# Performance work log

Measured on AMD Instinct MI355X. Metric: run time of the kernel, lower is better.

## Reference

```python
import jax, jax.numpy as jnp
import numpy as np

B, L, D = 16384, 50, 32  # batch, history length, embedding_dim
NU, NI, NC = 100000, 100000, 1000


def setup_inputs() -> dict:
    key = jax.random.key(0)
    ks = jax.random.split(key, 16)
    customer_id = jax.random.randint(ks[0], (B,), 0, NU)
    candidate_good = jax.random.randint(ks[1], (B,), 0, NI)
    candidate_class = jax.random.randint(ks[2], (B,), 0, NC)
    history_goods = jax.random.randint(ks[3], (B, L), 0, NI)
    history_classes = jax.random.randint(ks[4], (B, L), 0, NC)
    user_table = jax.random.normal(ks[5], (NU, D), jnp.float32) * 0.05
    item_table = jax.random.normal(ks[6], (NI, D), jnp.float32) * 0.05
    item_table = item_table.at[0].set(0.0)  # padding_idx=0
    cat_table = jax.random.normal(ks[7], (NC, D), jnp.float32) * 0.05
    cat_table = cat_table.at[0].set(0.0)  # padding_idx=0
    # attention net: Linear(4*2D=256 -> 80), Linear(80 -> 1)
    aw1 = jax.random.normal(ks[8], (4 * 2 * D, 80), jnp.float32) * 0.05
    ab1 = jnp.zeros((80,), jnp.float32)
    aw2 = jax.random.normal(ks[9], (80, 1), jnp.float32) * 0.05
    ab2 = jnp.zeros((1,), jnp.float32)
    # final mlp: 5D=160 -> 256 -> 128 -> 1
    mw1 = jax.random.normal(ks[10], (5 * D, 256), jnp.float32) * 0.05
    mb1 = jnp.zeros((256,), jnp.float32)
    mw2 = jax.random.normal(ks[11], (256, 128), jnp.float32) * 0.05
    mb2 = jnp.zeros((128,), jnp.float32)
    mw3 = jax.random.normal(ks[12], (128, 1), jnp.float32) * 0.05
    mb3 = jnp.zeros((1,), jnp.float32)
    return dict(customer_id=customer_id, candidate_good=candidate_good,
                candidate_class=candidate_class, history_goods=history_goods,
                history_classes=history_classes, user_table=user_table,
                item_table=item_table, cat_table=cat_table,
                aw1=aw1, ab1=ab1, aw2=aw2, ab2=ab2,
                mw1=mw1, mb1=mb1, mw2=mw2, mb2=mb2, mw3=mw3, mb3=mb3)


def reference(customer_id, candidate_good, candidate_class, history_goods,
              history_classes, user_table, item_table, cat_table,
              aw1, ab1, aw2, ab2, mw1, mb1, mw2, mb2, mw3, mb3):
    user_emb = user_table[customer_id]                               # [B, D]
    cand = jnp.concatenate([item_table[candidate_good],
                            cat_table[candidate_class]], axis=-1)    # [B, 2D]
    hist = jnp.concatenate([item_table[history_goods],
                            cat_table[history_classes]], axis=-1)    # [B, L, 2D]
    q = jnp.broadcast_to(cand[:, None, :], hist.shape)               # [B, L, 2D]
    info = jnp.concatenate([q, hist, q - hist, q * hist], axis=-1)   # [B, L, 8D]
    h = jax.nn.relu(info @ aw1 + ab1)                                # [B, L, 80]
    scores = (h @ aw2 + ab2)[..., 0]                                 # [B, L]
    mask = history_goods != 0
    scores = jnp.where(mask, scores, -1e9)
    weights = jax.nn.softmax(scores, axis=1)                         # [B, L]
    att = jnp.einsum('bl,bld->bd', weights, hist)                    # [B, 2D]
    combined = jnp.concatenate([user_emb, cand, att], axis=-1)       # [B, 5D]
    z = jax.nn.relu(combined @ mw1 + mb1)
    z = jax.nn.relu(z @ mw2 + mb2)
    out = (z @ mw3 + mb3)[..., 0]                                    # [B]
    return out
```

## Files before the change

### kernel.cpp

```cpp
#include <hip/hip_runtime.h>
#include <math.h>

#define LHIST 50

typedef __attribute__((ext_vector_type(8))) short bf16x8;
typedef __attribute__((ext_vector_type(4))) float f32x4;

__device__ __forceinline__ unsigned short f2bf(float f) {
    union { float f; unsigned u; } v; v.f = f;
    unsigned r = v.u + 0x7fff + ((v.u >> 16) & 1);
    return (unsigned short)(r >> 16);
}
__device__ __forceinline__ float bf2f(unsigned short h) {
    union { unsigned u; float f; } v; v.u = ((unsigned)h) << 16;
    return v.f;
}


__global__ void prep_kernel(const float* __restrict__ aw1,
                            const float* __restrict__ mw1,
                            const float* __restrict__ mw2,
                            const float* __restrict__ item_table,
                            const float* __restrict__ cat_table,
                            int itemN, int catN,
                            float* __restrict__ Awt,
                            unsigned short* __restrict__ Bmfb,
                            unsigned short* __restrict__ W4fb,
                            unsigned short* __restrict__ W1f,
                            unsigned short* __restrict__ W2f,
                            unsigned short* __restrict__ itemb,
                            unsigned short* __restrict__ catb) {
    int i = blockIdx.x * 256 + threadIdx.x;
    int i8 = i * 8;
    if (i8 + 7 < itemN) {
        float4 a = *(const float4*)&item_table[i8];
        float4 b = *(const float4*)&item_table[i8 + 4];
        ushort4 lo, hi;
        lo.x = f2bf(a.x); lo.y = f2bf(a.y); lo.z = f2bf(a.z); lo.w = f2bf(a.w);
        hi.x = f2bf(b.x); hi.y = f2bf(b.y); hi.z = f2bf(b.z); hi.w = f2bf(b.w);
        *(ushort4*)&itemb[i8] = lo;
        *(ushort4*)&itemb[i8 + 4] = hi;
    }
    if (i8 + 7 < catN) {
        float4 a = *(const float4*)&cat_table[i8];
        float4 b = *(const float4*)&cat_table[i8 + 4];
        ushort4 lo, hi;
        lo.x = f2bf(a.x); lo.y = f2bf(a.y); lo.z = f2bf(a.z); lo.w = f2bf(a.w);
        hi.x = f2bf(b.x); hi.y = f2bf(b.y); hi.z = f2bf(b.z); hi.w = f2bf(b.w);
        *(ushort4*)&catb[i8] = lo;
        *(ushort4*)&catb[i8 + 4] = hi;
    }
    if (i < 5120) {
        int j = i >> 6, k = i & 63;
        Awt[i] = aw1[k * 80 + j] + aw1[(128 + k) * 80 + j];
        int kk = i / 80, n = i - kk * 80;
        int nt = n >> 4, colw = n & 15, ks = kk >> 5, r = kk & 31, qd = r >> 3, off = r & 7;
        int d = ((nt * 2 + ks) * 64 + qd * 16 + colw) * 8 + off;
        Bmfb[d] = f2bf(aw1[(64 + kk) * 80 + n] - aw1[(128 + kk) * 80 + n]);
        W4fb[d] = f2bf(aw1[(192 + kk) * 80 + n]);
    }
    if (i < 40960) {
        int kk = i >> 8, n = i & 255;
        int nt = n >> 4, colw = n & 15, ks = kk >> 5, r = kk & 31, qd = r >> 3, off = r & 7;
        W1f[((nt * 5 + ks) * 64 + qd * 16 + colw) * 8 + off] = f2bf(mw1[i]);
    }
    if (i < 32768) {
        int kk = i >> 7, n = i & 127;
        int nt = n >> 4, colw = n & 15, ks = kk >> 5, r = kk & 31, qd = r >> 3, off = r & 7;
        W2f[((nt * 8 + ks) * 64 + qd * 16 + colw) * 8 + off] = f2bf(mw2[i]);
    }
}

__device__ __forceinline__ bf16x8 hq_frag(uint4 v, const float* qp) {
    union { uint4 u; unsigned short s[8]; } in; in.u = v;
    bf16x8 r;
    #pragma unroll
    for (int j = 0; j < 8; ++j) r[j] = (short)f2bf(bf2f(in.s[j]) * qp[j]);
    return r;
}

__global__ void __launch_bounds__(256, 4) attn_kernel(
    const int* __restrict__ cid, const int* __restrict__ cg,
    const int* __restrict__ cc,  const int* __restrict__ hg,
    const int* __restrict__ hc,
    const float* __restrict__ user_table, const float* __restrict__ item_table,
    const float* __restrict__ cat_table,
    const float* __restrict__ ab1, const float* __restrict__ aw2,
    const float* __restrict__ Awt, const unsigned short* __restrict__ Bmfb,
    const unsigned short* __restrict__ W4fb,
    const unsigned short* __restrict__ itemb, const unsigned short* __restrict__ catb,
    unsigned short* __restrict__ cfrag)
{
    __shared__ __align__(16) unsigned short sh_B[20 * 64 * 8];
    __shared__ __align__(16) float sh_q[4][64];
    __shared__ float sh_bias[4][80];
    __shared__ float sh_sc[4][64];
    __shared__ float sh_aw2[80];

    const int t = threadIdx.x;
    const int b0 = blockIdx.x * 4;
    const int wv = t >> 6;
    const int lane = t & 63;
    const int quad = lane >> 4;
    const int col = lane & 15;

    for (int i = t; i < 1280; i += 256) {
        int lane8 = i & 63;
        int ksnt = i >> 6;
        int nt = ksnt >> 2, ks = ksnt & 3;
        const unsigned short* src = (ks < 2)
            ? &Bmfb[((nt * 2 + ks) * 64 + lane8) * 8]
            : &W4fb[((nt * 2 + (ks - 2)) * 64 + lane8) * 8];
        *(uint4*)&sh_B[i * 8] = *(const uint4*)src;
    }
    {
        int qbi = wv;
        int b = b0 + qbi;
        float v = (lane < 32) ? item_table[(size_t)cg[b] * 32 + lane]
                              : cat_table[(size_t)cc[b] * 32 + (lane - 32)];
        sh_q[qbi][lane] = v;
    }
    if (t < 80) sh_aw2[t] = aw2[t];
    __syncthreads();

    const int b = b0 + wv;

    int il[4], ic[4];
    #pragma unroll
    for (int mt = 0; mt < 4; ++mt) {
        int l = mt * 16 + col;
        int lc = (l < LHIST) ? l : 0;
        il[mt] = hg[b * LHIST + lc];
        ic[mt] = hc[b * LHIST + lc];
    }
    uint4 vi0 = *(const uint4*)&itemb[(size_t)il[0] * 32 + quad * 8];
    uint4 vc0 = *(const uint4*)&catb[(size_t)ic[0] * 32 + quad * 8];
    uint4 vi1 = *(const uint4*)&itemb[(size_t)il[1] * 32 + quad * 8];
    uint4 vc1 = *(const uint4*)&catb[(size_t)ic[1] * 32 + quad * 8];

    for (int s = t; s < 320; s += 256) {
        int bi = s / 80, j = s - bi * 80;
        float acc = ab1[j];
        const float4* aw = (const float4*)&Awt[j * 64];
        #pragma unroll
        for (int k4 = 0; k4 < 16; ++k4) {
            float4 a = aw[k4];
            float4 q = *(const float4*)&sh_q[bi][k4 * 4];
            acc += a.x * q.x + a.y * q.y + a.z * q.z + a.w * q.w;
        }
        sh_bias[bi][j] = acc;
    }
    __syncthreads();

    float q0[8], q1[8];
    {
        float4 qa = *(const float4*)&sh_q[wv][quad * 8];
        float4 qb = *(const float4*)&sh_q[wv][quad * 8 + 4];
        q0[0]=qa.x; q0[1]=qa.y; q0[2]=qa.z; q0[3]=qa.w; q0[4]=qb.x; q0[5]=qb.y; q0[6]=qb.z; q0[7]=qb.w;
        float4 qc = *(const float4*)&sh_q[wv][32 + quad * 8];
        float4 qdv = *(const float4*)&sh_q[wv][32 + quad * 8 + 4];
        q1[0]=qc.x; q1[1]=qc.y; q1[2]=qc.z; q1[3]=qc.w; q1[4]=qdv.x; q1[5]=qdv.y; q1[6]=qdv.z; q1[7]=qdv.w;
    }
    float bias_v[5], a2_v[5];
    #pragma unroll
    for (int nt = 0; nt < 5; ++nt) {
        bias_v[nt] = sh_bias[wv][nt * 16 + col];
        a2_v[nt]   = sh_aw2[nt * 16 + col];
    }

    #pragma unroll
    for (int p = 0; p < 2; ++p) {
        bf16x8 afr[2][4];
        uint4 vi[2], vc[2];
        if (p == 0) { vi[0] = vi0; vc[0] = vc0; vi[1] = vi1; vc[1] = vc1; }
        else {
            vi[0] = *(const uint4*)&itemb[(size_t)il[2] * 32 + quad * 8];
            vc[0] = *(const uint4*)&catb[(size_t)ic[2] * 32 + quad * 8];
            vi[1] = *(const uint4*)&itemb[(size_t)il[3] * 32 + quad * 8];
            vc[1] = *(const uint4*)&catb[(size_t)ic[3] * 32 + quad * 8];
            if (48 + col >= LHIST) { vi[1] = make_uint4(0,0,0,0); vc[1] = make_uint4(0,0,0,0); }
        }
        #pragma unroll
        for (int mi = 0; mi < 2; ++mi) {
            afr[mi][0] = *(bf16x8*)&vi[mi];
            afr[mi][1] = *(bf16x8*)&vc[mi];
            afr[mi][2] = hq_frag(vi[mi], q0);
            afr[mi][3] = hq_frag(vc[mi], q1);
        }
        f32x4 acc[2][5];
        #pragma unroll
        for (int mi = 0; mi < 2; ++mi)
            #pragma unroll
            for (int nt = 0; nt < 5; ++nt) acc[mi][nt] = (f32x4){0.f,0.f,0.f,0.f};
        #pragma unroll
        for (int ks = 0; ks < 4; ++ks) {
            #pragma unroll
            for (int nt = 0; nt < 5; ++nt) {
                bf16x8 bfr = *(const bf16x8*)&sh_B[((nt * 4 + ks) * 64 + lane) * 8];
                acc[0][nt] = __builtin_amdgcn_mfma_f32_16x16x32_bf16(afr[0][ks], bfr, acc[0][nt], 0, 0, 0);
                acc[1][nt] = __builtin_amdgcn_mfma_f32_16x16x32_bf16(afr[1][ks], bfr, acc[1][nt], 0, 0, 0);
            }
        }
        #pragma unroll
        for (int mi = 0; mi < 2; ++mi) {
            int mt = p * 2 + mi;
            #pragma unroll
            for (int i = 0; i < 4; ++i) {
                float pp = 0.f;
                #pragma unroll
                for (int nt = 0; nt < 5; ++nt) {
                    float u = acc[mi][nt][i] + bias_v[nt];
                    pp += fmaxf(u, 0.f) * a2_v[nt];
                }
                pp += __shfl_xor(pp, 1);
                pp += __shfl_xor(pp, 2);
                pp += __shfl_xor(pp, 4);
                pp += __shfl_xor(pp, 8);
                if (col == 0) sh_sc[wv][mt * 16 + quad * 4 + i] = pp;
            }
        }
    }

    float sc = -INFINITY;
    if (lane < LHIST) {
        sc = sh_sc[wv][lane];
        if (hg[b * LHIST + lane] == 0) sc = -1e9f;
    }
    float m = sc;
    #pragma unroll
    for (int off = 32; off > 0; off >>= 1) m = fmaxf(m, __shfl_xor(m, off));
    float e = (lane < LHIST) ? __expf(sc - m) : 0.f;
    float ssum = e;
    #pragma unroll
    for (int off = 32; off > 0; off >>= 1) ssum += __shfl_xor(ssum, off);
    float w = e / ssum;

    int c = lane & 7, lgrp = lane >> 3;
    int isCat = c >> 2, s4 = c & 3;
    float at[8];
    #pragma unroll
    for (int j = 0; j < 8; ++j) at[j] = 0.f;
    #pragma unroll
    for (int it = 0; it < 7; ++it) {
        int l = it * 8 + lgrp;
        int lc = (l < LHIST) ? l : 0;
        float wl = __shfl(w, l);
        int idx = (isCat ? hc : hg)[b * LHIST + lc];
        uint4 hv = *(const uint4*)&(isCat ? catb : itemb)[(size_t)idx * 32 + s4 * 8];
        union { uint4 u; unsigned short s[8]; } hh; hh.u = hv;
        #pragma unroll
        for (int j = 0; j < 8; ++j) at[j] += wl * bf2f(hh.s[j]);
    }
    #pragma unroll
    for (int off = 8; off < 64; off <<= 1)
        #pragma unroll
        for (int j = 0; j < 8; ++j) at[j] += __shfl_xor(at[j], off);

    {
        int g = b >> 4, colm = b & 15;
        unsigned short* base = cfrag + (size_t)g * 2560;
        if (lane < 8) {
            int k0 = 96 + lane * 8;
            int ks = k0 >> 5, qd = (k0 >> 3) & 3;
            ushort4 lo, hi;
            lo.x = f2bf(at[0]); lo.y = f2bf(at[1]); lo.z = f2bf(at[2]); lo.w = f2bf(at[3]);
            hi.x = f2bf(at[4]); hi.y = f2bf(at[5]); hi.z = f2bf(at[6]); hi.w = f2bf(at[7]);
            unsigned short* p = base + ((ks * 64) + qd * 16 + colm) * 8;
            *(ushort4*)p = lo;
            *(ushort4*)(p + 4) = hi;
        } else if (lane < 16) {
            int cq = lane - 8;
            int k0 = 32 + cq * 8;
            int ks = k0 >> 5, qd = (k0 >> 3) & 3;
            float4 qa = *(const float4*)&sh_q[wv][cq * 8];
            float4 qb = *(const float4*)&sh_q[wv][cq * 8 + 4];
            ushort4 lo, hi;
            lo.x = f2bf(qa.x); lo.y = f2bf(qa.y); lo.z = f2bf(qa.z); lo.w = f2bf(qa.w);
            hi.x = f2bf(qb.x); hi.y = f2bf(qb.y); hi.z = f2bf(qb.z); hi.w = f2bf(qb.w);
            unsigned short* p = base + ((ks * 64) + qd * 16 + colm) * 8;
            *(ushort4*)p = lo;
            *(ushort4*)(p + 4) = hi;
        } else if (lane < 20) {
            int cu = lane - 16;
            int uidx = cid[b];
            float4 ua = *(const float4*)&user_table[(size_t)uidx * 32 + cu * 8];
            float4 ub = *(const float4*)&user_table[(size_t)uidx * 32 + cu * 8 + 4];
            ushort4 lo, hi;
            lo.x = f2bf(ua.x); lo.y = f2bf(ua.y); lo.z = f2bf(ua.z); lo.w = f2bf(ua.w);
            hi.x = f2bf(ub.x); hi.y = f2bf(ub.y); hi.z = f2bf(ub.z); hi.w = f2bf(ub.w);
            unsigned short* p = base + (cu * 16 + colm) * 8;
            *(ushort4*)p = lo;
            *(ushort4*)(p + 4) = hi;
        }
    }
}

__global__ void __launch_bounds__(256, 4) mlp_kernel(
    const unsigned short* __restrict__ cfrag,
    const unsigned short* __restrict__ W1f, const unsigned short* __restrict__ W2f,
    const float* __restrict__ mb1, const float* __restrict__ mb2,
    const float* __restrict__ mw3, const float* __restrict__ mb3,
    float* __restrict__ out)
{
    __shared__ __align__(16) unsigned short shA2[4096];
    __shared__ float sh_part[4][16];

    const int t = threadIdx.x;
    const int g = blockIdx.x;
    const int wv = t >> 6;
    const int lane = t & 63;
    const int quad = lane >> 4;
    const int col = lane & 15;
    const unsigned short* abase = cfrag + (size_t)g * 2560;

    f32x4 acc1[4];
    #pragma unroll
    for (int j = 0; j < 4; ++j) acc1[j] = (f32x4){0.f, 0.f, 0.f, 0.f};
    #pragma unroll
    for (int ks = 0; ks < 5; ++ks) {
        bf16x8 a = *(const bf16x8*)&abase[(ks * 64 + lane) * 8];
        #pragma unroll
        for (int j = 0; j < 4; ++j) {
            bf16x8 bw = *(const bf16x8*)&W1f[(((wv * 4 + j) * 5 + ks) * 64 + lane) * 8];
            acc1[j] = __builtin_amdgcn_mfma_f32_16x16x32_bf16(a, bw, acc1[j], 0, 0, 0);
        }
    }
    #pragma unroll
    for (int j = 0; j < 4; ++j) {
        int n = (wv * 4 + j) * 16 + col;
        float bj = mb1[n];
        int ks2 = n >> 5, qd2 = (n >> 3) & 3, off2 = n & 7;
        #pragma unroll
        for (int i = 0; i < 4; ++i) {
            float z = fmaxf(acc1[j][i] + bj, 0.f);
            shA2[(ks2 * 64 + qd2 * 16 + quad * 4 + i) * 8 + off2] = f2bf(z);
        }
    }
    __syncthreads();

    f32x4 acc2[2];
    #pragma unroll
    for (int jj = 0; jj < 2; ++jj) acc2[jj] = (f32x4){0.f, 0.f, 0.f, 0.f};
    #pragma unroll
    for (int ks = 0; ks < 8; ++ks) {
        bf16x8 a = *(const bf16x8*)&shA2[(ks * 64 + lane) * 8];
        #pragma unroll
        for (int jj = 0; jj < 2; ++jj) {
            bf16x8 bw = *(const bf16x8*)&W2f[(((wv * 2 + jj) * 8 + ks) * 64 + lane) * 8];
            acc2[jj] = __builtin_amdgcn_mfma_f32_16x16x32_bf16(a, bw, acc2[jj], 0, 0, 0);
        }
    }
    #pragma unroll
    for (int i = 0; i < 4; ++i) {
        float p = 0.f;
        #pragma unroll
        for (int jj = 0; jj < 2; ++jj) {
            int n = (wv * 2 + jj) * 16 + col;
            float z = fmaxf(acc2[jj][i] + mb2[n], 0.f);
            p += z * mw3[n];
        }
        p += __shfl_xor(p, 1);
        p += __shfl_xor(p, 2);
        p += __shfl_xor(p, 4);
        p += __shfl_xor(p, 8);
        if (col == 0) sh_part[wv][quad * 4 + i] = p;
    }
    __syncthreads();
    if (t < 16)
        out[g * 16 + t] = sh_part[0][t] + sh_part[1][t] + sh_part[2][t] + sh_part[3][t] + mb3[0];
}

extern "C" void kernel_launch(void* const* d_in, const int* in_sizes, int n_in,
                              void* d_out, int out_size, void* d_ws, size_t ws_size,
                              hipStream_t stream) {
    const int*   cid = (const int*)d_in[0];
    const int*   cg  = (const int*)d_in[1];
    const int*   cc  = (const int*)d_in[2];
    const int*   hg  = (const int*)d_in[3];
    const int*   hc  = (const int*)d_in[4];
    const float* user_table = (const float*)d_in[5];
    const float* item_table = (const float*)d_in[6];
    const float* cat_table  = (const float*)d_in[7];
    const float* aw1 = (const float*)d_in[8];
    const float* ab1 = (const float*)d_in[9];
    const float* aw2 = (const float*)d_in[10];
    const float* mw1 = (const float*)d_in[12];
    const float* mb1 = (const float*)d_in[13];
    const float* mw2 = (const float*)d_in[14];
    const float* mb2 = (const float*)d_in[15];
    const float* mw3 = (const float*)d_in[16];
    const float* mb3 = (const float*)d_in[17];
    float* out = (float*)d_out;

    const int B = in_sizes[0];
    const int itemN = in_sizes[6];
    const int catN  = in_sizes[7];
    float* ws = (float*)d_ws;
    float* Awt = ws;
    unsigned short* Bmfb = (unsigned short*)(ws + 5120);
    unsigned short* W4fb = (unsigned short*)(ws + 7680);
    unsigned short* W1f  = (unsigned short*)(ws + 10240);
    unsigned short* W2f  = (unsigned short*)(ws + 30720);
    unsigned short* itemb = (unsigned short*)(ws + 47104);
    unsigned short* catb  = itemb + itemN;
    unsigned short* cfrag = (unsigned short*)(ws + 47104 + (itemN + catN + 1) / 2);

    int n8 = (itemN + 7) / 8;
    int prep_grid = (n8 + 255) / 256;
    if (prep_grid < 160) prep_grid = 160;
    prep_kernel<<<prep_grid, 256, 0, stream>>>(aw1, mw1, mw2, item_table, cat_table,
                                               itemN, catN, Awt, Bmfb, W4fb, W1f, W2f,
                                               itemb, catb);
    attn_kernel<<<B / 4, 256, 0, stream>>>(cid, cg, cc, hg, hc,
                                           user_table, item_table, cat_table,
                                           ab1, aw2, Awt, Bmfb, W4fb, itemb, catb, cfrag);
    mlp_kernel<<<B / 16, 256, 0, stream>>>(cfrag, W1f, W2f,
                                           mb1, mb2, mw3, mb3, out);
}
```

Baseline: 197.6 us.

## Fold query into per-row B matrix, reuse history registers for attention sum

Instead of building q*hist A-fragments per element, each block forms a per-batch-row weight matrix (Bm + q∘W4) in shared memory, halving the MFMA K dimension from 4 to 2 k-steps. All four history fragment loads are issued up front and reused for the weighted-sum pooling, removing the second gather of history embeddings. bf16 packing uses 32-bit packed stores. Costs more LDS (4x5120 bf16) and register pressure from holding all fragments, and adds an extra bf16 rounding of the folded weights.

```diff
diff --git a/kernel.cpp b/kernel.cpp
--- a/kernel.cpp
+++ b/kernel.cpp
@@ -14,6 +14,9 @@
 __device__ __forceinline__ float bf2f(unsigned short h) {
     union { unsigned u; float f; } v; v.u = ((unsigned)h) << 16;
     return v.f;
+}
+__device__ __forceinline__ unsigned packbf2(float lo, float hi) {
+    return (unsigned)f2bf(lo) | ((unsigned)f2bf(hi) << 16);
 }
 
 
@@ -35,20 +38,18 @@
     if (i8 + 7 < itemN) {
         float4 a = *(const float4*)&item_table[i8];
         float4 b = *(const float4*)&item_table[i8 + 4];
-        ushort4 lo, hi;
-        lo.x = f2bf(a.x); lo.y = f2bf(a.y); lo.z = f2bf(a.z); lo.w = f2bf(a.w);
-        hi.x = f2bf(b.x); hi.y = f2bf(b.y); hi.z = f2bf(b.z); hi.w = f2bf(b.w);
-        *(ushort4*)&itemb[i8] = lo;
-        *(ushort4*)&itemb[i8 + 4] = hi;
+        uint4 r;
+        r.x = packbf2(a.x, a.y); r.y = packbf2(a.z, a.w);
+        r.z = packbf2(b.x, b.y); r.w = packbf2(b.z, b.w);
+        *(uint4*)&itemb[i8] = r;
     }
     if (i8 + 7 < catN) {
         float4 a = *(const float4*)&cat_table[i8];
         float4 b = *(const float4*)&cat_table[i8 + 4];
-        ushort4 lo, hi;
-        lo.x = f2bf(a.x); lo.y = f2bf(a.y); lo.z = f2bf(a.z); lo.w = f2bf(a.w);
-        hi.x = f2bf(b.x); hi.y = f2bf(b.y); hi.z = f2bf(b.z); hi.w = f2bf(b.w);
-        *(ushort4*)&catb[i8] = lo;
-        *(ushort4*)&catb[i8 + 4] = hi;
+        uint4 r;
+        r.x = packbf2(a.x, a.y); r.y = packbf2(a.z, a.w);
+        r.z = packbf2(b.x, b.y); r.w = packbf2(b.z, b.w);
+        *(uint4*)&catb[i8] = r;
     }
     if (i < 5120) {
         int j = i >> 6, k = i & 63;
@@ -69,14 +70,6 @@
         int nt = n >> 4, colw = n & 15, ks = kk >> 5, r = kk & 31, qd = r >> 3, off = r & 7;
         W2f[((nt * 8 + ks) * 64 + qd * 16 + colw) * 8 + off] = f2bf(mw2[i]);
     }
-}
-
-__device__ __forceinline__ bf16x8 hq_frag(uint4 v, const float* qp) {
-    union { uint4 u; unsigned short s[8]; } in; in.u = v;
-    bf16x8 r;
-    #pragma unroll
-    for (int j = 0; j < 8; ++j) r[j] = (short)f2bf(bf2f(in.s[j]) * qp[j]);
-    return r;
 }
 
 __global__ void __launch_bounds__(256, 4) attn_kernel(
@@ -91,11 +84,12 @@
     const unsigned short* __restrict__ itemb, const unsigned short* __restrict__ catb,
     unsigned short* __restrict__ cfrag)
 {
-    __shared__ __align__(16) unsigned short sh_B[20 * 64 * 8];
+    __shared__ __align__(16) unsigned short sh_Bq[4][5120];
     __shared__ __align__(16) float sh_q[4][64];
     __shared__ float sh_bias[4][80];
     __shared__ float sh_sc[4][64];
     __shared__ float sh_aw2[80];
+    __shared__ __align__(16) float sh_att[4][64];
 
     const int t = threadIdx.x;
     const int b0 = blockIdx.x * 4;
@@ -103,26 +97,6 @@
     const int lane = t & 63;
     const int quad = lane >> 4;
     const int col = lane & 15;
-
-    for (int i = t; i < 1280; i += 256) {
-        int lane8 = i & 63;
-        int ksnt = i >> 6;
-        int nt = ksnt >> 2, ks = ksnt & 3;
-        const unsigned short* src = (ks < 2)
-            ? &Bmfb[((nt * 2 + ks) * 64 + lane8) * 8]
-            : &W4fb[((nt * 2 + (ks - 2)) * 64 + lane8) * 8];
-        *(uint4*)&sh_B[i * 8] = *(const uint4*)src;
-    }
-    {
-        int qbi = wv;
-        int b = b0 + qbi;
-        float v = (lane < 32) ? item_table[(size_t)cg[b] * 32 + lane]
-                              : cat_table[(size_t)cc[b] * 32 + (lane - 32)];
-        sh_q[qbi][lane] = v;
-    }
-    if (t < 80) sh_aw2[t] = aw2[t];
-    __syncthreads();
-
     const int b = b0 + wv;
 
     int il[4], ic[4];
@@ -133,11 +107,44 @@
         il[mt] = hg[b * LHIST + lc];
         ic[mt] = hc[b * LHIST + lc];
     }
-    uint4 vi0 = *(const uint4*)&itemb[(size_t)il[0] * 32 + quad * 8];
-    uint4 vc0 = *(const uint4*)&catb[(size_t)ic[0] * 32 + quad * 8];
-    uint4 vi1 = *(const uint4*)&itemb[(size_t)il[1] * 32 + quad * 8];
-    uint4 vc1 = *(const uint4*)&catb[(size_t)ic[1] * 32 + quad * 8];
-
+    uint4 vi[4], vc[4];
+    #pragma unroll
+    for (int mt = 0; mt < 4; ++mt) {
+        vi[mt] = *(const uint4*)&itemb[(size_t)il[mt] * 32 + quad * 8];
+        vc[mt] = *(const uint4*)&catb[(size_t)ic[mt] * 32 + quad * 8];
+    }
+    {
+        float v = (lane < 32) ? item_table[(size_t)cg[b] * 32 + lane]
+                              : cat_table[(size_t)cc[b] * 32 + (lane - 32)];
+        sh_q[wv][lane] = v;
+    }
+    if (t < 80) sh_aw2[t] = aw2[t];
+    __syncthreads();
+
+    #pragma unroll
+    for (int it = 0; it < 10; ++it) {
+        int i = it * 256 + t;
+        int bb = i / 640;
+        int j = (i - bb * 640) * 8;
+        int lane8 = (j >> 3) & 63, ks = (j >> 9) & 1;
+        int kk = ks * 32 + (lane8 >> 4) * 8;
+        uint4 bm4 = *(const uint4*)&Bmfb[j];
+        uint4 w44 = *(const uint4*)&W4fb[j];
+        float4 qa = *(const float4*)&sh_q[bb][kk];
+        float4 qb = *(const float4*)&sh_q[bb][kk + 4];
+        unsigned bmw[4] = {bm4.x, bm4.y, bm4.z, bm4.w};
+        unsigned w4w[4] = {w44.x, w44.y, w44.z, w44.w};
+        float qv[8] = {qa.x, qa.y, qa.z, qa.w, qb.x, qb.y, qb.z, qb.w};
+        uint4 res;
+        unsigned* rp = (unsigned*)&res;
+        #pragma unroll
+        for (int d = 0; d < 4; ++d) {
+            float lo = bf2f((unsigned short)(bmw[d] & 0xffff)) + qv[2 * d]     * bf2f((unsigned short)(w4w[d] & 0xffff));
+            float hi = bf2f((unsigned short)(bmw[d] >> 16))    + qv[2 * d + 1] * bf2f((unsigned short)(w4w[d] >> 16));
+            rp[d] = packbf2(lo, hi);
+        }
+        *(uint4*)&sh_Bq[bb][j] = res;
+    }
     for (int s = t; s < 320; s += 256) {
         int bi = s / 80, j = s - bi * 80;
         float acc = ab1[j];
@@ -152,15 +159,6 @@
     }
     __syncthreads();
 
-    float q0[8], q1[8];
-    {
-        float4 qa = *(const float4*)&sh_q[wv][quad * 8];
-        float4 qb = *(const float4*)&sh_q[wv][quad * 8 + 4];
-        q0[0]=qa.x; q0[1]=qa.y; q0[2]=qa.z; q0[3]=qa.w; q0[4]=qb.x; q0[5]=qb.y; q0[6]=qb.z; q0[7]=qb.w;
-        float4 qc = *(const float4*)&sh_q[wv][32 + quad * 8];
-        float4 qdv = *(const float4*)&sh_q[wv][32 + quad * 8 + 4];
-        q1[0]=qc.x; q1[1]=qc.y; q1[2]=qc.z; q1[3]=qc.w; q1[4]=qdv.x; q1[5]=qdv.y; q1[6]=qdv.z; q1[7]=qdv.w;
-    }
     float bias_v[5], a2_v[5];
     #pragma unroll
     for (int nt = 0; nt < 5; ++nt) {
@@ -170,36 +168,23 @@
 
     #pragma unroll
     for (int p = 0; p < 2; ++p) {
-        bf16x8 afr[2][4];
-        uint4 vi[2], vc[2];
-        if (p == 0) { vi[0] = vi0; vc[0] = vc0; vi[1] = vi1; vc[1] = vc1; }
-        else {
-            vi[0] = *(const uint4*)&itemb[(size_t)il[2] * 32 + quad * 8];
-            vc[0] = *(const uint4*)&catb[(size_t)ic[2] * 32 + quad * 8];
-            vi[1] = *(const uint4*)&itemb[(size_t)il[3] * 32 + quad * 8];
-            vc[1] = *(const uint4*)&catb[(size_t)ic[3] * 32 + quad * 8];
-            if (48 + col >= LHIST) { vi[1] = make_uint4(0,0,0,0); vc[1] = make_uint4(0,0,0,0); }
-        }
-        #pragma unroll
-        for (int mi = 0; mi < 2; ++mi) {
-            afr[mi][0] = *(bf16x8*)&vi[mi];
-            afr[mi][1] = *(bf16x8*)&vc[mi];
-            afr[mi][2] = hq_frag(vi[mi], q0);
-            afr[mi][3] = hq_frag(vc[mi], q1);
-        }
         f32x4 acc[2][5];
         #pragma unroll
         for (int mi = 0; mi < 2; ++mi)
             #pragma unroll
             for (int nt = 0; nt < 5; ++nt) acc[mi][nt] = (f32x4){0.f,0.f,0.f,0.f};
-        #pragma unroll
-        for (int ks = 0; ks < 4; ++ks) {
-            #pragma unroll
-            for (int nt = 0; nt < 5; ++nt) {
-                bf16x8 bfr = *(const bf16x8*)&sh_B[((nt * 4 + ks) * 64 + lane) * 8];
-                acc[0][nt] = __builtin_amdgcn_mfma_f32_16x16x32_bf16(afr[0][ks], bfr, acc[0][nt], 0, 0, 0);
-                acc[1][nt] = __builtin_amdgcn_mfma_f32_16x16x32_bf16(afr[1][ks], bfr, acc[1][nt], 0, 0, 0);
-            }
+        bf16x8 a0i = *(bf16x8*)&vi[p * 2];
+        bf16x8 a0c = *(bf16x8*)&vc[p * 2];
+        bf16x8 a1i = *(bf16x8*)&vi[p * 2 + 1];
+        bf16x8 a1c = *(bf16x8*)&vc[p * 2 + 1];
+        #pragma unroll
+        for (int nt = 0; nt < 5; ++nt) {
+            bf16x8 b0 = *(const bf16x8*)&sh_Bq[wv][((nt * 2 + 0) * 64 + lane) * 8];
+            acc[0][nt] = __builtin_amdgcn_mfma_f32_16x16x32_bf16(a0i, b0, acc[0][nt], 0, 0, 0);
+            acc[1][nt] = __builtin_amdgcn_mfma_f32_16x16x32_bf16(a1i, b0, acc[1][nt], 0, 0, 0);
+            bf16x8 b1 = *(const bf16x8*)&sh_Bq[wv][((nt * 2 + 1) * 64 + lane) * 8];
+            acc[0][nt] = __builtin_amdgcn_mfma_f32_16x16x32_bf16(a0c, b1, acc[0][nt], 0, 0, 0);
+            acc[1][nt] = __builtin_amdgcn_mfma_f32_16x16x32_bf16(a1c, b1, acc[1][nt], 0, 0, 0);
         }
         #pragma unroll
         for (int mi = 0; mi < 2; ++mi) {
@@ -235,62 +220,71 @@
     for (int off = 32; off > 0; off >>= 1) ssum += __shfl_xor(ssum, off);
     float w = e / ssum;
 
-    int c = lane & 7, lgrp = lane >> 3;
-    int isCat = c >> 2, s4 = c & 3;
-    float at[8];
-    #pragma unroll
-    for (int j = 0; j < 8; ++j) at[j] = 0.f;
-    #pragma unroll
-    for (int it = 0; it < 7; ++it) {
-        int l = it * 8 + lgrp;
-        int lc = (l < LHIST) ? l : 0;
-        float wl = __shfl(w, l);
-        int idx = (isCat ? hc : hg)[b * LHIST + lc];
-        uint4 hv = *(const uint4*)&(isCat ? catb : itemb)[(size_t)idx * 32 + s4 * 8];
-        union { uint4 u; unsigned short s[8]; } hh; hh.u = hv;
-        #pragma unroll
-        for (int j = 0; j < 8; ++j) at[j] += wl * bf2f(hh.s[j]);
-    }
-    #pragma unroll
-    for (int off = 8; off < 64; off <<= 1)
-        #pragma unroll
-        for (int j = 0; j < 8; ++j) at[j] += __shfl_xor(at[j], off);
+    {
+        float wl[4];
+        wl[0] = __shfl(w, col);
+        wl[1] = __shfl(w, 16 + col);
+        wl[2] = __shfl(w, 32 + col);
+        wl[3] = __shfl(w, 48 + col);
+        float at0[8], at1[8];
+        #pragma unroll
+        for (int j = 0; j < 8; ++j) { at0[j] = 0.f; at1[j] = 0.f; }
+        #pragma unroll
+        for (int mt = 0; mt < 4; ++mt) {
+            union { uint4 u; unsigned short s[8]; } hi, hcv;
+            hi.u = vi[mt]; hcv.u = vc[mt];
+            #pragma unroll
+            for (int j = 0; j < 8; ++j) {
+                at0[j] += wl[mt] * bf2f(hi.s[j]);
+                at1[j] += wl[mt] * bf2f(hcv.s[j]);
+            }
+        }
+        #pragma unroll
+        for (int off = 1; off < 16; off <<= 1)
+            #pragma unroll
+            for (int j = 0; j < 8; ++j) {
+                at0[j] += __shfl_xor(at0[j], off);
+                at1[j] += __shfl_xor(at1[j], off);
+            }
+        if (col == 0) {
+            *(float4*)&sh_att[wv][quad * 8]     = make_float4(at0[0], at0[1], at0[2], at0[3]);
+            *(float4*)&sh_att[wv][quad * 8 + 4] = make_float4(at0[4], at0[5], at0[6], at0[7]);
+            *(float4*)&sh_att[wv][32 + quad * 8]     = make_float4(at1[0], at1[1], at1[2], at1[3]);
+            *(float4*)&sh_att[wv][32 + quad * 8 + 4] = make_float4(at1[4], at1[5], at1[6], at1[7]);
+        }
+    }
 
     {
         int g = b >> 4, colm = b & 15;
         unsigned short* base = cfrag + (size_t)g * 2560;
         if (lane < 8) {
+            float4 aa = *(const float4*)&sh_att[wv][lane * 8];
+            float4 ab = *(const float4*)&sh_att[wv][lane * 8 + 4];
             int k0 = 96 + lane * 8;
             int ks = k0 >> 5, qd = (k0 >> 3) & 3;
-            ushort4 lo, hi;
-            lo.x = f2bf(at[0]); lo.y = f2bf(at[1]); lo.z = f2bf(at[2]); lo.w = f2bf(at[3]);
-            hi.x = f2bf(at[4]); hi.y = f2bf(at[5]); hi.z = f2bf(at[6]); hi.w = f2bf(at[7]);
-            unsigned short* p = base + ((ks * 64) + qd * 16 + colm) * 8;
-            *(ushort4*)p = lo;
-            *(ushort4*)(p + 4) = hi;
+            uint4 r;
+            r.x = packbf2(aa.x, aa.y); r.y = packbf2(aa.z, aa.w);
+            r.z = packbf2(ab.x, ab.y); r.w = packbf2(ab.z, ab.w);
+            *(uint4*)(base + ((ks * 64) + qd * 16 + colm) * 8) = r;
         } else if (lane < 16) {
             int cq = lane - 8;
             int k0 = 32 + cq * 8;
             int ks = k0 >> 5, qd = (k0 >> 3) & 3;
             float4 qa = *(const float4*)&sh_q[wv][cq * 8];
             float4 qb = *(const float4*)&sh_q[wv][cq * 8 + 4];
-            ushort4 lo, hi;
-            lo.x = f2bf(qa.x); lo.y = f2bf(qa.y); lo.z = f2bf(qa.z); lo.w = f2bf(qa.w);
-            hi.x = f2bf(qb.x); hi.y = f2bf(qb.y); hi.z = f2bf(qb.z); hi.w = f2bf(qb.w);
-            unsigned short* p = base + ((ks * 64) + qd * 16 + colm) * 8;
-            *(ushort4*)p = lo;
-            *(ushort4*)(p + 4) = hi;
+            uint4 r;
+            r.x = packbf2(qa.x, qa.y); r.y = packbf2(qa.z, qa.w);
+            r.z = packbf2(qb.x, qb.y); r.w = packbf2(qb.z, qb.w);
+            *(uint4*)(base + ((ks * 64) + qd * 16 + colm) * 8) = r;
         } else if (lane < 20) {
             int cu = lane - 16;
             int uidx = cid[b];
             float4 ua = *(const float4*)&user_table[(size_t)uidx * 32 + cu * 8];
             float4 ub = *(const float4*)&user_table[(size_t)uidx * 32 + cu * 8 + 4];
-            ushort4 lo, hi;
-            lo.x = f2bf(ua.x); lo.y = f2bf(ua.y); lo.z = f2bf(ua.z); lo.w = f2bf(ua.w);
-            hi.x = f2bf(ub.x); hi.y = f2bf(ub.y); hi.z = f2bf(ub.z); hi.w = f2bf(ub.w);
-            unsigned short* p = base + (cu * 16 + colm) * 8;
-            *(ushort4*)p = lo;
-            *(ushort4*)(p + 4) = hi;
+            uint4 r;
+            r.x = packbf2(ua.x, ua.y); r.y = packbf2(ua.z, ua.w);
+            r.z = packbf2(ub.x, ub.y); r.w = packbf2(ub.z, ub.w);
+            *(uint4*)(base + (cu * 16 + colm) * 8) = r;
         }
     }
 }
```

Result: slower. 211.5 us (+7.0%).
